# Kernel optimization log

Hardware: AMD Instinct MI355X
Metric: run time of the kernel (lower is better)

The kernel has to match this reference:

```python
import jax, jax.numpy as jnp
import numpy as np

D = 2048        # input_size / model dim
H = 2816        # hidden_size per expert (GLU -> w1 has 2*H rows)
E = 8           # num_experts
M = 4096        # tokens (batch*seq)


def setup_inputs() -> dict:
    key = jax.random.key(0)
    k1, k2, k3, k4, k5 = jax.random.split(key, 5)
    x = jax.random.normal(k1, (M, D), dtype=jnp.float32)
    # ParallelExperts init: uniform(-1/fan_in_dim, 1/fan_in_dim); scale kept simple here
    w1 = jax.random.uniform(k2, (E, 2 * H, D), dtype=jnp.float32, minval=-1.0, maxval=1.0) / (2 * H)
    w2 = jax.random.uniform(k3, (E, D, H), dtype=jnp.float32, minval=-1.0, maxval=1.0) / D
    router_w = jax.random.normal(k4, (E, D), dtype=jnp.float32) * (1.0 / np.sqrt(D))
    bias = jnp.zeros((D,), dtype=jnp.float32)
    return {"x": x, "w1": w1, "w2": w2, "router_w": router_w, "bias": bias, "top_k": 2}


def _moe_forward(x, w1, w2, router_w, bias, top_k):
    # Router: logits -> softmax (fp32) -> top-k -> renormalize (fused_moe semantics)
    logits = x @ router_w.T                                # [M, E]
    probs = jax.nn.softmax(logits.astype(jnp.float32), axis=-1)
    topk_w, topk_ids = jax.lax.top_k(probs, top_k)         # [M, k]
    topk_w = topk_w / jnp.sum(topk_w, axis=-1, keepdims=True)
    # Dense combine weights [M, E]: gate weight if expert selected, else 0
    m = x.shape[0]
    combine = jnp.zeros((m, w1.shape[0]), dtype=x.dtype)
    combine = combine.at[jnp.arange(m)[:, None], topk_ids].add(topk_w.astype(x.dtype))
    # Grouped expert GEMMs, expressed as a loop over the small fixed expert set.
    # Contribution of expert e is masked by combine[:, e] (zero for unrouted tokens).
    y = jnp.zeros_like(x)
    hdim = w2.shape[2]
    for e in range(w1.shape[0]):
        g = x @ w1[e].T                                    # [M, 2H]
        h = jax.nn.silu(g[:, :hdim]) * g[:, hdim:]          # silu_and_mul (GLU)
        y = y + combine[:, e:e + 1] * (h @ w2[e].T)         # [M, D]
    return y + bias


def reference(x, w1, w2, router_w, bias, top_k):
    return _moe_forward(x, w1, w2, router_w, bias, top_k)
```

## Files before the change

kernel.cpp:

```cpp
#include <hip/hip_runtime.h>
#include <hip/hip_bf16.h>
#include <stdint.h>

#define M_TOK 4096
#define DDIM  2048
#define HDIM  2816
#define NEXP  8
#define PMAX  10240
#define MAXTILES 40
#define NB1   22
#define NB2   8
#define NT1   64
#define NT2   88

typedef __attribute__((ext_vector_type(8))) short short8;
typedef __attribute__((ext_vector_type(4))) float f32x4;

#define GLD16(g, l) __builtin_amdgcn_global_load_lds(                              \
    (const __attribute__((address_space(1))) unsigned int*)(g),                    \
    (__attribute__((address_space(3))) unsigned int*)(l), 16, 0, 0)

#define VMCNT(n) asm volatile("s_waitcnt vmcnt(" #n ")" ::: "memory")

__device__ __forceinline__ unsigned short f2bf(float f) {
  unsigned int u = __float_as_uint(f);
  u += 0x7fffu + ((u >> 16) & 1u);
  return (unsigned short)(u >> 16);
}
__device__ __forceinline__ float bf2f(unsigned short u) {
  return __uint_as_float(((unsigned)u) << 16);
}

#define PHASE(TT, VM, STG)                                                       \
  {                                                                              \
    VMCNT(VM);                                                                   \
    __builtin_amdgcn_s_barrier();                                                \
    asm volatile("" ::: "memory");                                               \
    if (STG) {                                                                   \
      int st_ = (TT) + 3;                                                        \
      int t4s_ = st_ & 3;                                                        \
      size_t kb_ = (size_t)st_ * 64;                                             \
      GLD16(aS0 + kb_, ldsp + t4s_ * 16384 + aD0);                               \
      GLD16(aS1 + kb_, ldsp + t4s_ * 16384 + aD1);                               \
      GLD16(bS0 + kb_, ldsp + 65536 + t4s_ * 16384 + aD0);                       \
      GLD16(bS1 + kb_, ldsp + 65536 + t4s_ * 16384 + aD1);                       \
    }                                                                            \
    {                                                                            \
      int t4_ = (TT) & 3;                                                        \
      const char* ab_ = ldsp + t4_ * 16384;                                      \
      const char* bb_ = ldsp + 65536 + t4_ * 16384;                              \
      short8 av_[8], bv_[4];                                                     \
      _Pragma("unroll") for (int mi = 0; mi < 8; ++mi)                           \
        av_[mi] = *(const short8*)(ab_ + aoff[mi]);                              \
      _Pragma("unroll") for (int ni = 0; ni < 4; ++ni)                           \
        bv_[ni] = *(const short8*)(bb_ + boff[ni]);                              \
      __builtin_amdgcn_s_setprio(1);                                             \
      _Pragma("unroll") for (int mi = 0; mi < 8; ++mi)                           \
        _Pragma("unroll") for (int ni = 0; ni < 4; ++ni)                         \
          acc[mi][ni] = __builtin_amdgcn_mfma_f32_16x16x32_bf16(av_[mi], bv_[ni], acc[mi][ni], 0, 0, 0); \
      __builtin_amdgcn_s_setprio(0);                                             \
    }                                                                            \
  }

__global__ void cvt_bf16_k(const float4* __restrict__ in, ushort4* __restrict__ out, int n4) {
  int stride = gridDim.x * blockDim.x;
  for (int i = blockIdx.x * blockDim.x + threadIdx.x; i < n4; i += stride) {
    float4 v = in[i];
    ushort4 o;
    o.x = f2bf(v.x); o.y = f2bf(v.y); o.z = f2bf(v.z); o.w = f2bf(v.w);
    out[i] = o;
  }
}

__global__ void init_k(int* __restrict__ tok, int* __restrict__ counts, int* __restrict__ cursors) {
  int i = blockIdx.x * blockDim.x + threadIdx.x;
  if (i < PMAX) tok[i] = -1;
  if (i < NEXP) { counts[i] = 0; cursors[i] = 0; }
}

__global__ __launch_bounds__(256) void router_k(const float* __restrict__ x,
                                                const float* __restrict__ rw,
                                                float* __restrict__ wgt,
                                                int* __restrict__ eid,
                                                int* __restrict__ counts) {
  int lane = threadIdx.x & 63;
  int wv = threadIdx.x >> 6;
  int t = blockIdx.x * 4 + wv;
  const float* xr = x + (size_t)t * DDIM;
  float acc[NEXP];
#pragma unroll
  for (int e = 0; e < NEXP; ++e) acc[e] = 0.f;
  for (int j = 0; j < DDIM / 64; ++j) {
    float xv = xr[lane + j * 64];
#pragma unroll
    for (int e = 0; e < NEXP; ++e) acc[e] += xv * rw[e * DDIM + lane + j * 64];
  }
#pragma unroll
  for (int e = 0; e < NEXP; ++e) {
#pragma unroll
    for (int s = 32; s > 0; s >>= 1) acc[e] += __shfl_xor(acc[e], s, 64);
  }
  if (lane == 0) {
    float mx = acc[0];
#pragma unroll
    for (int e = 1; e < NEXP; ++e) mx = fmaxf(mx, acc[e]);
    float p[NEXP];
#pragma unroll
    for (int e = 0; e < NEXP; ++e) p[e] = expf(acc[e] - mx);
    int e0 = 0; float p0 = p[0];
#pragma unroll
    for (int e = 1; e < NEXP; ++e) if (p[e] > p0) { p0 = p[e]; e0 = e; }
    int e1 = -1; float p1 = -1.f;
#pragma unroll
    for (int e = 0; e < NEXP; ++e) if (e != e0 && p[e] > p1) { p1 = p[e]; e1 = e; }
    float s = p0 + p1;
    wgt[2 * t] = p0 / s; wgt[2 * t + 1] = p1 / s;
    eid[2 * t] = e0;     eid[2 * t + 1] = e1;
    atomicAdd(&counts[e0], 1);
    atomicAdd(&counts[e1], 1);
  }
}

__global__ void offsets_k(const int* __restrict__ counts, int* __restrict__ offs,
                          int* __restrict__ tile2exp, int* __restrict__ tilerow,
                          int* __restrict__ ntiles) {
  if (threadIdx.x == 0 && blockIdx.x == 0) {
    int o = 0, nt = 0;
    for (int e = 0; e < NEXP; ++e) {
      offs[e] = o;
      int c = counts[e];
      int pt = (c + 255) >> 8;
      for (int i = 0; i < pt; ++i) { tile2exp[nt] = e; tilerow[nt] = o + i * 256; ++nt; }
      o += pt << 8;
    }
    offs[NEXP] = o;
    ntiles[0] = nt;
  }
}

__global__ void scatter_k(const int* __restrict__ eid, const int* __restrict__ offs,
                          int* __restrict__ cursors, int* __restrict__ tok,
                          int* __restrict__ slot) {
  int t = blockIdx.x * blockDim.x + threadIdx.x;
  if (t >= M_TOK) return;
#pragma unroll
  for (int k = 0; k < 2; ++k) {
    int e = eid[2 * t + k];
    int p = offs[e] + atomicAdd(&cursors[e], 1);
    tok[p] = t;
    slot[2 * t + k] = p;
  }
}

__global__ __launch_bounds__(512, 2) void gemm1_k(const unsigned short* __restrict__ xb,
                                                  const unsigned short* __restrict__ w1b,
                                                  const int* __restrict__ tok,
                                                  const int* __restrict__ tile2exp,
                                                  const int* __restrict__ tilerow,
                                                  const int* __restrict__ ntiles,
                                                  unsigned short* __restrict__ h) {
  __shared__ char ldsp[131072];
  int mt = blockIdx.x;
  if (mt >= ntiles[0]) return;
  int e = tile2exp[mt], r0 = tilerow[mt];
  int n0 = blockIdx.y * 128;
  int tid = threadIdx.x, lane = tid & 63;
  int wv = tid >> 6, wm = wv >> 2, wn = wv & 3;
  int l15 = lane & 15, g = lane >> 4;

  int row0 = tid >> 2, g0 = (tid & 3) ^ ((row0 >> 1) & 3);
  int s1i = 512 + tid;
  int row1 = s1i >> 2, g1 = (s1i & 3) ^ ((row1 >> 1) & 3);
  int t0 = tok[r0 + row0]; if (t0 < 0) t0 = 0;
  int t1 = tok[r0 + row1]; if (t1 < 0) t1 = 0;
  const char* aS0 = (const char*)xb + (size_t)t0 * (DDIM * 2) + g0 * 16;
  const char* aS1 = (const char*)xb + (size_t)t1 * (DDIM * 2) + g1 * 16;
  size_t w1r0 = (size_t)e * (2 * HDIM) +
                (row0 < 128 ? (size_t)(n0 + row0) : (size_t)(HDIM + n0 + row0 - 128));
  size_t w1r1 = (size_t)e * (2 * HDIM) +
                (row1 < 128 ? (size_t)(n0 + row1) : (size_t)(HDIM + n0 + row1 - 128));
  const char* bS0 = (const char*)w1b + w1r0 * (DDIM * 2) + g0 * 16;
  const char* bS1 = (const char*)w1b + w1r1 * (DDIM * 2) + g1 * 16;
  int aD0 = tid * 16, aD1 = 8192 + tid * 16;

  int aoff[8], boff[4];
#pragma unroll
  for (int mi = 0; mi < 8; ++mi) {
    int r = wm * 128 + mi * 16 + l15;
    aoff[mi] = r * 64 + ((g ^ ((r >> 1) & 3)) * 16);
  }
#pragma unroll
  for (int ni = 0; ni < 4; ++ni) {
    int r = wn * 64 + ni * 16 + l15;
    boff[ni] = r * 64 + ((g ^ ((r >> 1) & 3)) * 16);
  }

  f32x4 acc[8][4];
#pragma unroll
  for (int mi = 0; mi < 8; ++mi)
#pragma unroll
    for (int ni = 0; ni < 4; ++ni) acc[mi][ni] = (f32x4)(0.f);

#pragma unroll
  for (int t = 0; t < 3; ++t) {
    GLD16(aS0 + (size_t)t * 64, ldsp + t * 16384 + aD0);
    GLD16(aS1 + (size_t)t * 64, ldsp + t * 16384 + aD1);
    GLD16(bS0 + (size_t)t * 64, ldsp + 65536 + t * 16384 + aD0);
    GLD16(bS1 + (size_t)t * 64, ldsp + 65536 + t * 16384 + aD1);
  }

  int T = 0;
  for (; T + 3 < NT1; ++T) PHASE(T, 8, 1);
  PHASE(T, 8, 0); ++T;
  PHASE(T, 4, 0); ++T;
  PHASE(T, 0, 0);

  __syncthreads();
  float* xch = (float*)ldsp;
  int rbase = (lane >> 4) * 4;
  if (wn >= 2) {
    int uc0 = (wn - 2) * 64;
#pragma unroll
    for (int mi = 0; mi < 8; ++mi)
#pragma unroll
      for (int ni = 0; ni < 4; ++ni)
#pragma unroll
        for (int j = 0; j < 4; ++j) {
          int r = wm * 128 + mi * 16 + rbase + j;
          int c = uc0 + ni * 16 + l15;
          xch[r * 128 + c] = acc[mi][ni][j];
        }
  }
  __syncthreads();
  if (wn < 2) {
#pragma unroll
    for (int mi = 0; mi < 8; ++mi)
#pragma unroll
      for (int ni = 0; ni < 4; ++ni)
#pragma unroll
        for (int j = 0; j < 4; ++j) {
          int r = wm * 128 + mi * 16 + rbase + j;
          int c = wn * 64 + ni * 16 + l15;
          float gg = acc[mi][ni][j];
          float u = xch[r * 128 + c];
          float sv = gg / (1.f + expf(-gg));
          h[(size_t)(r0 + r) * HDIM + n0 + c] = f2bf(sv * u);
        }
  }
}

__global__ __launch_bounds__(512, 2) void gemm2_k(const unsigned short* __restrict__ h,
                                                  const unsigned short* __restrict__ w2b,
                                                  const int* __restrict__ tile2exp,
                                                  const int* __restrict__ tilerow,
                                                  const int* __restrict__ ntiles,
                                                  unsigned short* __restrict__ yp) {
  __shared__ char ldsp[131072];
  int mt = blockIdx.x;
  if (mt >= ntiles[0]) return;
  int e = tile2exp[mt], r0 = tilerow[mt];
  int n0 = blockIdx.y * 256;
  int tid = threadIdx.x, lane = tid & 63;
  int wv = tid >> 6, wm = wv >> 2, wn = wv & 3;
  int l15 = lane & 15, g = lane >> 4;

  int row0 = tid >> 2, g0 = (tid & 3) ^ ((row0 >> 1) & 3);
  int s1i = 512 + tid;
  int row1 = s1i >> 2, g1 = (s1i & 3) ^ ((row1 >> 1) & 3);
  const char* aS0 = (const char*)h + (size_t)(r0 + row0) * (HDIM * 2) + g0 * 16;
  const char* aS1 = (const char*)h + (size_t)(r0 + row1) * (HDIM * 2) + g1 * 16;
  const char* bS0 = (const char*)w2b + ((size_t)e * DDIM + n0 + row0) * (HDIM * 2) + g0 * 16;
  const char* bS1 = (const char*)w2b + ((size_t)e * DDIM + n0 + row1) * (HDIM * 2) + g1 * 16;
  int aD0 = tid * 16, aD1 = 8192 + tid * 16;

  int aoff[8], boff[4];
#pragma unroll
  for (int mi = 0; mi < 8; ++mi) {
    int r = wm * 128 + mi * 16 + l15;
    aoff[mi] = r * 64 + ((g ^ ((r >> 1) & 3)) * 16);
  }
#pragma unroll
  for (int ni = 0; ni < 4; ++ni) {
    int r = wn * 64 + ni * 16 + l15;
    boff[ni] = r * 64 + ((g ^ ((r >> 1) & 3)) * 16);
  }

  f32x4 acc[8][4];
#pragma unroll
  for (int mi = 0; mi < 8; ++mi)
#pragma unroll
    for (int ni = 0; ni < 4; ++ni) acc[mi][ni] = (f32x4)(0.f);

#pragma unroll
  for (int t = 0; t < 3; ++t) {
    GLD16(aS0 + (size_t)t * 64, ldsp + t * 16384 + aD0);
    GLD16(aS1 + (size_t)t * 64, ldsp + t * 16384 + aD1);
    GLD16(bS0 + (size_t)t * 64, ldsp + 65536 + t * 16384 + aD0);
    GLD16(bS1 + (size_t)t * 64, ldsp + 65536 + t * 16384 + aD1);
  }

  int T = 0;
  for (; T + 3 < NT2; ++T) PHASE(T, 8, 1);
  PHASE(T, 8, 0); ++T;
  PHASE(T, 4, 0); ++T;
  PHASE(T, 0, 0);

  int rbase = (lane >> 4) * 4;
#pragma unroll
  for (int mi = 0; mi < 8; ++mi)
#pragma unroll
    for (int ni = 0; ni < 4; ++ni)
#pragma unroll
      for (int j = 0; j < 4; ++j) {
        int r = r0 + wm * 128 + mi * 16 + rbase + j;
        int c = n0 + wn * 64 + ni * 16 + l15;
        yp[(size_t)r * DDIM + c] = f2bf(acc[mi][ni][j]);
      }
}

__global__ void combine_k(const unsigned short* __restrict__ yp, const float* __restrict__ wgt,
                          const int* __restrict__ slot, const float* __restrict__ bias,
                          float* __restrict__ out) {
  int idx = blockIdx.x * blockDim.x + threadIdx.x;
  int t = idx >> 8, q = (idx & 255) * 8;
  float w0 = wgt[2 * t], w1 = wgt[2 * t + 1];
  int s0 = slot[2 * t], s1 = slot[2 * t + 1];
  short8 a8 = *(const short8*)(yp + (size_t)s0 * DDIM + q);
  short8 b8 = *(const short8*)(yp + (size_t)s1 * DDIM + q);
  float* op = out + (size_t)t * DDIM + q;
#pragma unroll
  for (int k = 0; k < 8; ++k) {
    float av = bf2f((unsigned short)a8[k]);
    float bv = bf2f((unsigned short)b8[k]);
    op[k] = w0 * av + w1 * bv + bias[q + k];
  }
}

extern "C" void kernel_launch(void* const* d_in, const int* in_sizes, int n_in,
                              void* d_out, int out_size, void* d_ws, size_t ws_size,
                              hipStream_t stream) {
  const float* x    = (const float*)d_in[0];
  const float* w1   = (const float*)d_in[1];
  const float* w2   = (const float*)d_in[2];
  const float* rw   = (const float*)d_in[3];
  const float* bias = (const float*)d_in[4];
  float* out = (float*)d_out;

  char* ws = (char*)d_ws;
  size_t off = 0;
  auto alloc = [&](size_t bytes) -> void* {
    void* p = ws + off;
    off = (off + bytes + 255) & ~(size_t)255;
    return p;
  };
  unsigned short* w1b = (unsigned short*)alloc((size_t)NEXP * 2 * HDIM * DDIM * 2);
  unsigned short* w2b = (unsigned short*)alloc((size_t)NEXP * DDIM * HDIM * 2);
  unsigned short* xb  = (unsigned short*)alloc((size_t)M_TOK * DDIM * 2);
  unsigned short* h   = (unsigned short*)alloc((size_t)PMAX * HDIM * 2);
  unsigned short* yp  = (unsigned short*)alloc((size_t)PMAX * DDIM * 2);
  float* wgt          = (float*)alloc((size_t)M_TOK * 2 * 4);
  int* eid            = (int*)alloc((size_t)M_TOK * 2 * 4);
  int* slot           = (int*)alloc((size_t)M_TOK * 2 * 4);
  int* tok            = (int*)alloc((size_t)PMAX * 4);
  int* counts         = (int*)alloc(64 * 4);
  int* cursors        = (int*)alloc(64 * 4);
  int* offs           = (int*)alloc(64 * 4);
  int* ntiles         = (int*)alloc(64 * 4);
  int* tile2exp       = (int*)alloc(128 * 4);
  int* tilerow        = (int*)alloc(128 * 4);

  hipLaunchKernelGGL(init_k, dim3((PMAX + 255) / 256), dim3(256), 0, stream, tok, counts, cursors);
  hipLaunchKernelGGL(cvt_bf16_k, dim3(2048), dim3(256), 0, stream,
                     (const float4*)w1, (ushort4*)w1b, (int)((size_t)NEXP * 2 * HDIM * DDIM / 4));
  hipLaunchKernelGGL(cvt_bf16_k, dim3(2048), dim3(256), 0, stream,
                     (const float4*)w2, (ushort4*)w2b, (int)((size_t)NEXP * DDIM * HDIM / 4));
  hipLaunchKernelGGL(cvt_bf16_k, dim3(2048), dim3(256), 0, stream,
                     (const float4*)x, (ushort4*)xb, (int)((size_t)M_TOK * DDIM / 4));
  hipLaunchKernelGGL(router_k, dim3(M_TOK / 4), dim3(256), 0, stream, x, rw, wgt, eid, counts);
  hipLaunchKernelGGL(offsets_k, dim3(1), dim3(64), 0, stream, counts, offs, tile2exp, tilerow, ntiles);
  hipLaunchKernelGGL(scatter_k, dim3((M_TOK + 255) / 256), dim3(256), 0, stream, eid, offs, cursors, tok, slot);
  hipLaunchKernelGGL(gemm1_k, dim3(MAXTILES, NB1), dim3(512), 0, stream, xb, w1b, tok, tile2exp, tilerow, ntiles, h);
  hipLaunchKernelGGL(gemm2_k, dim3(MAXTILES, NB2), dim3(512), 0, stream, h, w2b, tile2exp, tilerow, ntiles, yp);
  hipLaunchKernelGGL(combine_k, dim3(M_TOK * (DDIM / 8) / 256), dim3(256), 0, stream, yp, wgt, slot, bias, out);
}
```

Baseline: 763.5 us.

## Fuse x conversion into router, overlap w2 conversion with gemm1, retile gemm2

The router kernel now writes the bf16 copy of x itself, which removes a separate conversion pass over x. The fp32-to-bf16 conversion of w2 moves into extra blocks of the gemm1 grid so it runs alongside the first GEMM. Both GEMMs get register double-buffered LDS reads under a sched_barrier, and occupancy drops to one block per CU. gemm2 uses 128-row tiles, giving twice as many tiles and less LDS per block. The gemm1 epilogue exchange buffer gets an XOR swizzle to reduce bank conflicts. The risks are that the conversion blocks compete with GEMM blocks for CUs and that the lower occupancy cannot hide latency as well.

Result: no change. 752.0 us (-1.5%).

```diff
diff --git a/kernel.cpp b/kernel.cpp
--- a/kernel.cpp
+++ b/kernel.cpp
@@ -8,7 +8,9 @@
 #define NEXP  8
 #define PMAX  10240
 #define MAXTILES 40
+#define CVW   8
 #define NB1   22
+#define MAXT2 80
 #define NB2   8
 #define NT1   64
 #define NT2   88
@@ -30,37 +32,6 @@
 __device__ __forceinline__ float bf2f(unsigned short u) {
   return __uint_as_float(((unsigned)u) << 16);
 }
-
-#define PHASE(TT, VM, STG)                                                       \
-  {                                                                              \
-    VMCNT(VM);                                                                   \
-    __builtin_amdgcn_s_barrier();                                                \
-    asm volatile("" ::: "memory");                                               \
-    if (STG) {                                                                   \
-      int st_ = (TT) + 3;                                                        \
-      int t4s_ = st_ & 3;                                                        \
-      size_t kb_ = (size_t)st_ * 64;                                             \
-      GLD16(aS0 + kb_, ldsp + t4s_ * 16384 + aD0);                               \
-      GLD16(aS1 + kb_, ldsp + t4s_ * 16384 + aD1);                               \
-      GLD16(bS0 + kb_, ldsp + 65536 + t4s_ * 16384 + aD0);                       \
-      GLD16(bS1 + kb_, ldsp + 65536 + t4s_ * 16384 + aD1);                       \
-    }                                                                            \
-    {                                                                            \
-      int t4_ = (TT) & 3;                                                        \
-      const char* ab_ = ldsp + t4_ * 16384;                                      \
-      const char* bb_ = ldsp + 65536 + t4_ * 16384;                              \
-      short8 av_[8], bv_[4];                                                     \
-      _Pragma("unroll") for (int mi = 0; mi < 8; ++mi)                           \
-        av_[mi] = *(const short8*)(ab_ + aoff[mi]);                              \
-      _Pragma("unroll") for (int ni = 0; ni < 4; ++ni)                           \
-        bv_[ni] = *(const short8*)(bb_ + boff[ni]);                              \
-      __builtin_amdgcn_s_setprio(1);                                             \
-      _Pragma("unroll") for (int mi = 0; mi < 8; ++mi)                           \
-        _Pragma("unroll") for (int ni = 0; ni < 4; ++ni)                         \
-          acc[mi][ni] = __builtin_amdgcn_mfma_f32_16x16x32_bf16(av_[mi], bv_[ni], acc[mi][ni], 0, 0, 0); \
-      __builtin_amdgcn_s_setprio(0);                                             \
-    }                                                                            \
-  }
 
 __global__ void cvt_bf16_k(const float4* __restrict__ in, ushort4* __restrict__ out, int n4) {
   int stride = gridDim.x * blockDim.x;
@@ -78,22 +49,30 @@
   if (i < NEXP) { counts[i] = 0; cursors[i] = 0; }
 }
 
-__global__ __launch_bounds__(256) void router_k(const float* __restrict__ x,
-                                                const float* __restrict__ rw,
+__global__ __launch_bounds__(256) void router_k(const float4* __restrict__ x4,
+                                                const float4* __restrict__ rw4,
+                                                ushort4* __restrict__ xb4,
                                                 float* __restrict__ wgt,
                                                 int* __restrict__ eid,
                                                 int* __restrict__ counts) {
   int lane = threadIdx.x & 63;
   int wv = threadIdx.x >> 6;
   int t = blockIdx.x * 4 + wv;
-  const float* xr = x + (size_t)t * DDIM;
+  int base = t * (DDIM / 4);
   float acc[NEXP];
 #pragma unroll
   for (int e = 0; e < NEXP; ++e) acc[e] = 0.f;
-  for (int j = 0; j < DDIM / 64; ++j) {
-    float xv = xr[lane + j * 64];
-#pragma unroll
-    for (int e = 0; e < NEXP; ++e) acc[e] += xv * rw[e * DDIM + lane + j * 64];
+#pragma unroll
+  for (int j = 0; j < DDIM / 4 / 64; ++j) {
+    float4 v = x4[base + j * 64 + lane];
+    ushort4 o;
+    o.x = f2bf(v.x); o.y = f2bf(v.y); o.z = f2bf(v.z); o.w = f2bf(v.w);
+    xb4[base + j * 64 + lane] = o;
+#pragma unroll
+    for (int e = 0; e < NEXP; ++e) {
+      float4 w = rw4[e * (DDIM / 4) + j * 64 + lane];
+      acc[e] += v.x * w.x + v.y * w.y + v.z * w.z + v.w * w.w;
+    }
   }
 #pragma unroll
   for (int e = 0; e < NEXP; ++e) {
@@ -123,18 +102,25 @@
 
 __global__ void offsets_k(const int* __restrict__ counts, int* __restrict__ offs,
                           int* __restrict__ tile2exp, int* __restrict__ tilerow,
-                          int* __restrict__ ntiles) {
+                          int* __restrict__ ntiles,
+                          int* __restrict__ tile2exp2, int* __restrict__ tilerow2,
+                          int* __restrict__ ntiles2) {
   if (threadIdx.x == 0 && blockIdx.x == 0) {
-    int o = 0, nt = 0;
+    int o = 0, nt = 0, nt2 = 0;
     for (int e = 0; e < NEXP; ++e) {
       offs[e] = o;
       int c = counts[e];
       int pt = (c + 255) >> 8;
-      for (int i = 0; i < pt; ++i) { tile2exp[nt] = e; tilerow[nt] = o + i * 256; ++nt; }
+      for (int i = 0; i < pt; ++i) {
+        tile2exp[nt] = e; tilerow[nt] = o + i * 256; ++nt;
+        tile2exp2[nt2] = e; tilerow2[nt2] = o + i * 256; ++nt2;
+        tile2exp2[nt2] = e; tilerow2[nt2] = o + i * 256 + 128; ++nt2;
+      }
       o += pt << 8;
     }
     offs[NEXP] = o;
     ntiles[0] = nt;
+    ntiles2[0] = nt2;
   }
 }
 
@@ -152,15 +138,62 @@
   }
 }
 
-__global__ __launch_bounds__(512, 2) void gemm1_k(const unsigned short* __restrict__ xb,
+#define STAGE1(TT)                                                               \
+  { size_t kb_ = (size_t)(TT) * 64;                                              \
+    char* d_ = ldsp + ((TT) & 3) * 16384;                                        \
+    GLD16(aS0 + kb_, d_ + aD0);                                                  \
+    GLD16(aS1 + kb_, d_ + aD1);                                                  \
+    GLD16(bS0 + kb_, d_ + 65536 + aD0);                                          \
+    GLD16(bS1 + kb_, d_ + 65536 + aD1); }
+
+#define DSRD1(TT, AV, BV)                                                        \
+  { const char* ab_ = ldsp + ((TT) & 3) * 16384;                                 \
+    const char* bb_ = ab_ + 65536;                                               \
+    _Pragma("unroll") for (int mi = 0; mi < 8; ++mi)                             \
+      AV[mi] = *(const short8*)(ab_ + aoff[mi]);                                 \
+    _Pragma("unroll") for (int ni = 0; ni < 4; ++ni)                             \
+      BV[ni] = *(const short8*)(bb_ + boff[ni]); }
+
+#define MMA1(AV, BV)                                                             \
+  { __builtin_amdgcn_s_setprio(1);                                               \
+    _Pragma("unroll") for (int mi = 0; mi < 8; ++mi)                             \
+      _Pragma("unroll") for (int ni = 0; ni < 4; ++ni)                           \
+        acc[mi][ni] = __builtin_amdgcn_mfma_f32_16x16x32_bf16(AV[mi], BV[ni], acc[mi][ni], 0, 0, 0); \
+    __builtin_amdgcn_s_setprio(0); }
+
+#define BODY1(TT, VMN, STG, AVC, BVC, AVN, BVN, RD)                              \
+  { VMCNT(VMN);                                                                  \
+    __builtin_amdgcn_s_barrier();                                                \
+    asm volatile("" ::: "memory");                                               \
+    if (STG) STAGE1((TT) + 3);                                                   \
+    if (RD) DSRD1((TT) + 1, AVN, BVN);                                           \
+    __builtin_amdgcn_sched_barrier(0);                                           \
+    MMA1(AVC, BVC); }
+
+__global__ __launch_bounds__(512, 1) void gemm1_k(const unsigned short* __restrict__ xb,
                                                   const unsigned short* __restrict__ w1b,
                                                   const int* __restrict__ tok,
                                                   const int* __restrict__ tile2exp,
                                                   const int* __restrict__ tilerow,
                                                   const int* __restrict__ ntiles,
-                                                  unsigned short* __restrict__ h) {
+                                                  unsigned short* __restrict__ h,
+                                                  const float4* __restrict__ w2src,
+                                                  ushort4* __restrict__ w2b4) {
   __shared__ char ldsp[131072];
-  int mt = blockIdx.x;
+  int bx = blockIdx.x;
+  if (bx >= MAXTILES) {
+    int id = (bx - MAXTILES) * NB1 + blockIdx.y;
+    const int n4 = NEXP * DDIM * HDIM / 4;
+    const int stride = CVW * NB1 * 512;
+    for (int i = id * 512 + threadIdx.x; i < n4; i += stride) {
+      float4 v = w2src[i];
+      ushort4 o;
+      o.x = f2bf(v.x); o.y = f2bf(v.y); o.z = f2bf(v.z); o.w = f2bf(v.w);
+      w2b4[i] = o;
+    }
+    return;
+  }
+  int mt = bx;
   if (mt >= ntiles[0]) return;
   int e = tile2exp[mt], r0 = tilerow[mt];
   int n0 = blockIdx.y * 128;
@@ -201,19 +234,24 @@
 #pragma unroll
     for (int ni = 0; ni < 4; ++ni) acc[mi][ni] = (f32x4)(0.f);
 
-#pragma unroll
-  for (int t = 0; t < 3; ++t) {
-    GLD16(aS0 + (size_t)t * 64, ldsp + t * 16384 + aD0);
-    GLD16(aS1 + (size_t)t * 64, ldsp + t * 16384 + aD1);
-    GLD16(bS0 + (size_t)t * 64, ldsp + 65536 + t * 16384 + aD0);
-    GLD16(bS1 + (size_t)t * 64, ldsp + 65536 + t * 16384 + aD1);
-  }
-
-  int T = 0;
-  for (; T + 3 < NT1; ++T) PHASE(T, 8, 1);
-  PHASE(T, 8, 0); ++T;
-  PHASE(T, 4, 0); ++T;
-  PHASE(T, 0, 0);
+  short8 avA[8], bvA[4], avB[8], bvB[4];
+
+  STAGE1(0); STAGE1(1); STAGE1(2);
+  VMCNT(8);
+  __builtin_amdgcn_s_barrier();
+  asm volatile("" ::: "memory");
+  DSRD1(0, avA, bvA);
+
+  for (int T = 0; T < NT1 - 4; T += 4) {
+    BODY1(T + 0, 4, 1, avA, bvA, avB, bvB, 1);
+    BODY1(T + 1, 4, 1, avB, bvB, avA, bvA, 1);
+    BODY1(T + 2, 4, 1, avA, bvA, avB, bvB, 1);
+    BODY1(T + 3, 4, 1, avB, bvB, avA, bvA, 1);
+  }
+  BODY1(NT1 - 4, 4, 1, avA, bvA, avB, bvB, 1);
+  BODY1(NT1 - 3, 4, 0, avB, bvB, avA, bvA, 1);
+  BODY1(NT1 - 2, 0, 0, avA, bvA, avB, bvB, 1);
+  BODY1(NT1 - 1, 0, 0, avB, bvB, avA, bvA, 0);
 
   __syncthreads();
   float* xch = (float*)ldsp;
@@ -228,7 +266,8 @@
         for (int j = 0; j < 4; ++j) {
           int r = wm * 128 + mi * 16 + rbase + j;
           int c = uc0 + ni * 16 + l15;
-          xch[r * 128 + c] = acc[mi][ni][j];
+          int cs = c ^ ((r & 3) << 2) ^ ((r & 1) << 4);
+          xch[r * 128 + cs] = acc[mi][ni][j];
         }
   }
   __syncthreads();
@@ -241,42 +280,73 @@
         for (int j = 0; j < 4; ++j) {
           int r = wm * 128 + mi * 16 + rbase + j;
           int c = wn * 64 + ni * 16 + l15;
+          int cs = c ^ ((r & 3) << 2) ^ ((r & 1) << 4);
           float gg = acc[mi][ni][j];
-          float u = xch[r * 128 + c];
+          float u = xch[r * 128 + cs];
           float sv = gg / (1.f + expf(-gg));
           h[(size_t)(r0 + r) * HDIM + n0 + c] = f2bf(sv * u);
         }
   }
 }
 
-__global__ __launch_bounds__(512, 2) void gemm2_k(const unsigned short* __restrict__ h,
+#define STAGE2(TT)                                                               \
+  { size_t kb_ = (size_t)(TT) * 64;                                              \
+    GLD16(aS0 + kb_, ldsp + ((TT) & 3) * 8192 + aD0);                            \
+    GLD16(bS0 + kb_, ldsp + 32768 + ((TT) & 3) * 16384 + bD0);                   \
+    GLD16(bS1 + kb_, ldsp + 32768 + ((TT) & 3) * 16384 + bD1); }
+
+#define DSRD2(TT, AV, BV)                                                        \
+  { const char* ab_ = ldsp + ((TT) & 3) * 8192;                                  \
+    const char* bb_ = ldsp + 32768 + ((TT) & 3) * 16384;                         \
+    _Pragma("unroll") for (int mi = 0; mi < 4; ++mi)                             \
+      AV[mi] = *(const short8*)(ab_ + aoff[mi]);                                 \
+    _Pragma("unroll") for (int ni = 0; ni < 4; ++ni)                             \
+      BV[ni] = *(const short8*)(bb_ + boff[ni]); }
+
+#define MMA2(AV, BV)                                                             \
+  { __builtin_amdgcn_s_setprio(1);                                               \
+    _Pragma("unroll") for (int mi = 0; mi < 4; ++mi)                             \
+      _Pragma("unroll") for (int ni = 0; ni < 4; ++ni)                           \
+        acc[mi][ni] = __builtin_amdgcn_mfma_f32_16x16x32_bf16(AV[mi], BV[ni], acc[mi][ni], 0, 0, 0); \
+    __builtin_amdgcn_s_setprio(0); }
+
+#define BODY2(TT, VMN, STG, AVC, BVC, AVN, BVN, RD)                              \
+  { VMCNT(VMN);                                                                  \
+    __builtin_amdgcn_s_barrier();                                                \
+    asm volatile("" ::: "memory");                                               \
+    if (STG) STAGE2((TT) + 3);                                                   \
+    if (RD) DSRD2((TT) + 1, AVN, BVN);                                           \
+    __builtin_amdgcn_sched_barrier(0);                                           \
+    MMA2(AVC, BVC); }
+
+__global__ __launch_bounds__(512, 1) void gemm2_k(const unsigned short* __restrict__ h,
                                                   const unsigned short* __restrict__ w2b,
-                                                  const int* __restrict__ tile2exp,
-                                                  const int* __restrict__ tilerow,
-                                                  const int* __restrict__ ntiles,
+                                                  const int* __restrict__ tile2exp2,
+                                                  const int* __restrict__ tilerow2,
+                                                  const int* __restrict__ ntiles2,
                                                   unsigned short* __restrict__ yp) {
-  __shared__ char ldsp[131072];
+  __shared__ char ldsp[98304];
   int mt = blockIdx.x;
-  if (mt >= ntiles[0]) return;
-  int e = tile2exp[mt], r0 = tilerow[mt];
+  if (mt >= ntiles2[0]) return;
+  int e = tile2exp2[mt], r0 = tilerow2[mt];
   int n0 = blockIdx.y * 256;
   int tid = threadIdx.x, lane = tid & 63;
   int wv = tid >> 6, wm = wv >> 2, wn = wv & 3;
   int l15 = lane & 15, g = lane >> 4;
 
-  int row0 = tid >> 2, g0 = (tid & 3) ^ ((row0 >> 1) & 3);
+  int rowa = tid >> 2, ga = (tid & 3) ^ ((rowa >> 1) & 3);
+  int rb0 = tid >> 2, gb0 = (tid & 3) ^ ((rb0 >> 1) & 3);
   int s1i = 512 + tid;
-  int row1 = s1i >> 2, g1 = (s1i & 3) ^ ((row1 >> 1) & 3);
-  const char* aS0 = (const char*)h + (size_t)(r0 + row0) * (HDIM * 2) + g0 * 16;
-  const char* aS1 = (const char*)h + (size_t)(r0 + row1) * (HDIM * 2) + g1 * 16;
-  const char* bS0 = (const char*)w2b + ((size_t)e * DDIM + n0 + row0) * (HDIM * 2) + g0 * 16;
-  const char* bS1 = (const char*)w2b + ((size_t)e * DDIM + n0 + row1) * (HDIM * 2) + g1 * 16;
-  int aD0 = tid * 16, aD1 = 8192 + tid * 16;
-
-  int aoff[8], boff[4];
-#pragma unroll
-  for (int mi = 0; mi < 8; ++mi) {
-    int r = wm * 128 + mi * 16 + l15;
+  int rb1 = s1i >> 2, gb1 = (s1i & 3) ^ ((rb1 >> 1) & 3);
+  const char* aS0 = (const char*)h + (size_t)(r0 + rowa) * (HDIM * 2) + ga * 16;
+  const char* bS0 = (const char*)w2b + ((size_t)e * DDIM + n0 + rb0) * (HDIM * 2) + gb0 * 16;
+  const char* bS1 = (const char*)w2b + ((size_t)e * DDIM + n0 + rb1) * (HDIM * 2) + gb1 * 16;
+  int aD0 = tid * 16, bD0 = tid * 16, bD1 = 8192 + tid * 16;
+
+  int aoff[4], boff[4];
+#pragma unroll
+  for (int mi = 0; mi < 4; ++mi) {
+    int r = wm * 64 + mi * 16 + l15;
     aoff[mi] = r * 64 + ((g ^ ((r >> 1) & 3)) * 16);
   }
 #pragma unroll
@@ -285,34 +355,39 @@
     boff[ni] = r * 64 + ((g ^ ((r >> 1) & 3)) * 16);
   }
 
-  f32x4 acc[8][4];
-#pragma unroll
-  for (int mi = 0; mi < 8; ++mi)
+  f32x4 acc[4][4];
+#pragma unroll
+  for (int mi = 0; mi < 4; ++mi)
 #pragma unroll
     for (int ni = 0; ni < 4; ++ni) acc[mi][ni] = (f32x4)(0.f);
 
-#pragma unroll
-  for (int t = 0; t < 3; ++t) {
-    GLD16(aS0 + (size_t)t * 64, ldsp + t * 16384 + aD0);
-    GLD16(aS1 + (size_t)t * 64, ldsp + t * 16384 + aD1);
-    GLD16(bS0 + (size_t)t * 64, ldsp + 65536 + t * 16384 + aD0);
-    GLD16(bS1 + (size_t)t * 64, ldsp + 65536 + t * 16384 + aD1);
-  }
-
-  int T = 0;
-  for (; T + 3 < NT2; ++T) PHASE(T, 8, 1);
-  PHASE(T, 8, 0); ++T;
-  PHASE(T, 4, 0); ++T;
-  PHASE(T, 0, 0);
+  short8 avA[4], bvA[4], avB[4], bvB[4];
+
+  STAGE2(0); STAGE2(1); STAGE2(2);
+  VMCNT(6);
+  __builtin_amdgcn_s_barrier();
+  asm volatile("" ::: "memory");
+  DSRD2(0, avA, bvA);
+
+  for (int T = 0; T < NT2 - 4; T += 4) {
+    BODY2(T + 0, 3, 1, avA, bvA, avB, bvB, 1);
+    BODY2(T + 1, 3, 1, avB, bvB, avA, bvA, 1);
+    BODY2(T + 2, 3, 1, avA, bvA, avB, bvB, 1);
+    BODY2(T + 3, 3, 1, avB, bvB, avA, bvA, 1);
+  }
+  BODY2(NT2 - 4, 3, 1, avA, bvA, avB, bvB, 1);
+  BODY2(NT2 - 3, 3, 0, avB, bvB, avA, bvA, 1);
+  BODY2(NT2 - 2, 0, 0, avA, bvA, avB, bvB, 1);
+  BODY2(NT2 - 1, 0, 0, avB, bvB, avA, bvA, 0);
 
   int rbase = (lane >> 4) * 4;
 #pragma unroll
-  for (int mi = 0; mi < 8; ++mi)
+  for (int mi = 0; mi < 4; ++mi)
 #pragma unroll
     for (int ni = 0; ni < 4; ++ni)
 #pragma unroll
       for (int j = 0; j < 4; ++j) {
-        int r = r0 + wm * 128 + mi * 16 + rbase + j;
+        int r = r0 + wm * 64 + mi * 16 + rbase + j;
         int c = n0 + wn * 64 + ni * 16 + l15;
         yp[(size_t)r * DDIM + c] = f2bf(acc[mi][ni][j]);
       }
@@ -366,20 +441,23 @@
   int* cursors        = (int*)alloc(64 * 4);
   int* offs           = (int*)alloc(64 * 4);
   int* ntiles         = (int*)alloc(64 * 4);
+  int* ntiles2        = (int*)alloc(64 * 4);
   int* tile2exp       = (int*)alloc(128 * 4);
   int* tilerow        = (int*)alloc(128 * 4);
+  int* tile2exp2      = (int*)alloc(128 * 4);
+  int* tilerow2       = (int*)alloc(128 * 4);
 
   hipLaunchKernelGGL(init_k, dim3((PMAX + 255) / 256), dim3(256), 0, stream, tok, counts, cursors);
   hipLaunchKernelGGL(cvt_bf16_k, dim3(2048), dim3(256), 0, stream,
                      (const float4*)w1, (ushort4*)w1b, (int)((size_t)NEXP * 2 * HDIM * DDIM / 4));
-  hipLaunchKernelGGL(cvt_bf16_k, dim3(2048), dim3(256), 0, stream,
-                     (const float4*)w2, (ushort4*)w2b, (int)((size_t)NEXP * DDIM * HDIM / 4));
-  hipLaunchKernelGGL(cvt_bf16_k, dim3(2048), dim3(256), 0, stream,
-                     (const float4*)x, (ushort4*)xb, (int)((size_t)M_TOK * DDIM / 4));
-  hipLaunchKernelGGL(router_k, dim3(M_TOK / 4), dim3(256), 0, stream, x, rw, wgt, eid, counts);
-  hipLaunchKernelGGL(offsets_k, dim3(1), dim3(64), 0, stream, counts, offs, tile2exp, tilerow, ntiles);
+  hipLaunchKernelGGL(router_k, dim3(M_TOK / 4), dim3(256), 0, stream,
+                     (const float4*)x, (const float4*)rw, (ushort4*)xb, wgt, eid, counts);
+  hipLaunchKernelGGL(offsets_k, dim3(1), dim3(64), 0, stream, counts, offs,
+                     tile2exp, tilerow, ntiles, tile2exp2, tilerow2, ntiles2);
   hipLaunchKernelGGL(scatter_k, dim3((M_TOK + 255) / 256), dim3(256), 0, stream, eid, offs, cursors, tok, slot);
-  hipLaunchKernelGGL(gemm1_k, dim3(MAXTILES, NB1), dim3(512), 0, stream, xb, w1b, tok, tile2exp, tilerow, ntiles, h);
-  hipLaunchKernelGGL(gemm2_k, dim3(MAXTILES, NB2), dim3(512), 0, stream, h, w2b, tile2exp, tilerow, ntiles, yp);
+  hipLaunchKernelGGL(gemm1_k, dim3(MAXTILES + CVW, NB1), dim3(512), 0, stream,
+                     xb, w1b, tok, tile2exp, tilerow, ntiles, h, (const float4*)w2, (ushort4*)w2b);
+  hipLaunchKernelGGL(gemm2_k, dim3(MAXT2, NB2), dim3(512), 0, stream,
+                     h, w2b, tile2exp2, tilerow2, ntiles2, yp);
   hipLaunchKernelGGL(combine_k, dim3(M_TOK * (DDIM / 8) / 256), dim3(256), 0, stream, yp, wgt, slot, bias, out);
 }
```

## Split GEMM k-steps into two half-phases, fuse x cast into router, swizzle exchange

Applied to the files above, without the earlier changes.

Each GEMM k-step is split into two barrier-separated half-phases. The first loads half the A fragments and all B fragments and issues the A prefetch. The second loads the other A half and issues the B prefetch. This interleaves global-to-LDS traffic with MFMA work and cuts live fragment registers, while launch bounds drop to one block per SM. The separate x-to-bf16 conversion kernel is folded into the router kernel, which now reads float4, saving a full pass over x. The GLU exchange buffer in LDS gets an XOR column swizzle to reduce bank conflicts, at the cost of twice as many barriers per k-step.

Result: no change. 757.2 us (-0.8%).

```diff
diff --git a/kernel.cpp b/kernel.cpp
--- a/kernel.cpp
+++ b/kernel.cpp
@@ -31,36 +31,45 @@
   return __uint_as_float(((unsigned)u) << 16);
 }
 
-#define PHASE(TT, VM, STG)                                                       \
-  {                                                                              \
-    VMCNT(VM);                                                                   \
+#define GP0(KT, VM, STG)                                                         \
+  { VMCNT(VM);                                                                   \
     __builtin_amdgcn_s_barrier();                                                \
     asm volatile("" ::: "memory");                                               \
-    if (STG) {                                                                   \
-      int st_ = (TT) + 3;                                                        \
-      int t4s_ = st_ & 3;                                                        \
-      size_t kb_ = (size_t)st_ * 64;                                             \
-      GLD16(aS0 + kb_, ldsp + t4s_ * 16384 + aD0);                               \
-      GLD16(aS1 + kb_, ldsp + t4s_ * 16384 + aD1);                               \
-      GLD16(bS0 + kb_, ldsp + 65536 + t4s_ * 16384 + aD0);                       \
-      GLD16(bS1 + kb_, ldsp + 65536 + t4s_ * 16384 + aD1);                       \
+    { const char* ab_ = ldsp + ((KT) & 3) * 16384;                               \
+      const char* bb_ = ldsp + 65536 + ((KT) & 3) * 16384;                       \
+      _Pragma("unroll") for (int mi = 0; mi < 4; ++mi)                           \
+        av[mi] = *(const short8*)(ab_ + aoff[mi]);                               \
+      _Pragma("unroll") for (int ni = 0; ni < 4; ++ni)                           \
+        bv[ni] = *(const short8*)(bb_ + boff[ni]);                               \
+      if (STG) { size_t kb_ = (size_t)((KT) + 3) * 64;                           \
+        char* d_ = ldsp + (((KT) + 3) & 3) * 16384;                              \
+        GLD16(aS0 + kb_, d_ + aD0); GLD16(aS1 + kb_, d_ + aD1); }                \
     }                                                                            \
-    {                                                                            \
-      int t4_ = (TT) & 3;                                                        \
-      const char* ab_ = ldsp + t4_ * 16384;                                      \
-      const char* bb_ = ldsp + 65536 + t4_ * 16384;                              \
-      short8 av_[8], bv_[4];                                                     \
-      _Pragma("unroll") for (int mi = 0; mi < 8; ++mi)                           \
-        av_[mi] = *(const short8*)(ab_ + aoff[mi]);                              \
+    asm volatile("" ::: "memory");                                               \
+    __builtin_amdgcn_s_barrier();                                                \
+    __builtin_amdgcn_s_setprio(1);                                               \
+    _Pragma("unroll") for (int mi = 0; mi < 4; ++mi)                             \
       _Pragma("unroll") for (int ni = 0; ni < 4; ++ni)                           \
-        bv_[ni] = *(const short8*)(bb_ + boff[ni]);                              \
-      __builtin_amdgcn_s_setprio(1);                                             \
-      _Pragma("unroll") for (int mi = 0; mi < 8; ++mi)                           \
-        _Pragma("unroll") for (int ni = 0; ni < 4; ++ni)                         \
-          acc[mi][ni] = __builtin_amdgcn_mfma_f32_16x16x32_bf16(av_[mi], bv_[ni], acc[mi][ni], 0, 0, 0); \
-      __builtin_amdgcn_s_setprio(0);                                             \
+        acc[mi][ni] = __builtin_amdgcn_mfma_f32_16x16x32_bf16(av[mi], bv[ni], acc[mi][ni], 0, 0, 0); \
+    __builtin_amdgcn_s_setprio(0); }
+
+#define GP1(KT, STG)                                                             \
+  { __builtin_amdgcn_s_barrier();                                                \
+    asm volatile("" ::: "memory");                                               \
+    { const char* ab_ = ldsp + ((KT) & 3) * 16384;                               \
+      _Pragma("unroll") for (int mi = 0; mi < 4; ++mi)                           \
+        av[mi] = *(const short8*)(ab_ + aoff[4 + mi]);                           \
+      if (STG) { size_t kb_ = (size_t)((KT) + 3) * 64;                           \
+        char* d_ = ldsp + 65536 + (((KT) + 3) & 3) * 16384;                      \
+        GLD16(bS0 + kb_, d_ + aD0); GLD16(bS1 + kb_, d_ + aD1); }                \
     }                                                                            \
-  }
+    asm volatile("" ::: "memory");                                               \
+    __builtin_amdgcn_s_barrier();                                                \
+    __builtin_amdgcn_s_setprio(1);                                               \
+    _Pragma("unroll") for (int mi = 0; mi < 4; ++mi)                             \
+      _Pragma("unroll") for (int ni = 0; ni < 4; ++ni)                           \
+        acc[4 + mi][ni] = __builtin_amdgcn_mfma_f32_16x16x32_bf16(av[mi], bv[ni], acc[4 + mi][ni], 0, 0, 0); \
+    __builtin_amdgcn_s_setprio(0); }
 
 __global__ void cvt_bf16_k(const float4* __restrict__ in, ushort4* __restrict__ out, int n4) {
   int stride = gridDim.x * blockDim.x;
@@ -78,22 +87,30 @@
   if (i < NEXP) { counts[i] = 0; cursors[i] = 0; }
 }
 
-__global__ __launch_bounds__(256) void router_k(const float* __restrict__ x,
-                                                const float* __restrict__ rw,
+__global__ __launch_bounds__(256) void router_k(const float4* __restrict__ x4,
+                                                const float4* __restrict__ rw4,
+                                                ushort4* __restrict__ xb4,
                                                 float* __restrict__ wgt,
                                                 int* __restrict__ eid,
                                                 int* __restrict__ counts) {
   int lane = threadIdx.x & 63;
   int wv = threadIdx.x >> 6;
   int t = blockIdx.x * 4 + wv;
-  const float* xr = x + (size_t)t * DDIM;
+  int base = t * (DDIM / 4);
   float acc[NEXP];
 #pragma unroll
   for (int e = 0; e < NEXP; ++e) acc[e] = 0.f;
-  for (int j = 0; j < DDIM / 64; ++j) {
-    float xv = xr[lane + j * 64];
-#pragma unroll
-    for (int e = 0; e < NEXP; ++e) acc[e] += xv * rw[e * DDIM + lane + j * 64];
+#pragma unroll
+  for (int j = 0; j < DDIM / 4 / 64; ++j) {
+    float4 v = x4[base + j * 64 + lane];
+    ushort4 o;
+    o.x = f2bf(v.x); o.y = f2bf(v.y); o.z = f2bf(v.z); o.w = f2bf(v.w);
+    xb4[base + j * 64 + lane] = o;
+#pragma unroll
+    for (int e = 0; e < NEXP; ++e) {
+      float4 w = rw4[e * (DDIM / 4) + j * 64 + lane];
+      acc[e] += v.x * w.x + v.y * w.y + v.z * w.z + v.w * w.w;
+    }
   }
 #pragma unroll
   for (int e = 0; e < NEXP; ++e) {
@@ -152,7 +169,7 @@
   }
 }
 
-__global__ __launch_bounds__(512, 2) void gemm1_k(const unsigned short* __restrict__ xb,
+__global__ __launch_bounds__(512, 1) void gemm1_k(const unsigned short* __restrict__ xb,
                                                   const unsigned short* __restrict__ w1b,
                                                   const int* __restrict__ tok,
                                                   const int* __restrict__ tile2exp,
@@ -169,18 +186,16 @@
   int l15 = lane & 15, g = lane >> 4;
 
   int row0 = tid >> 2, g0 = (tid & 3) ^ ((row0 >> 1) & 3);
-  int s1i = 512 + tid;
-  int row1 = s1i >> 2, g1 = (s1i & 3) ^ ((row1 >> 1) & 3);
+  int row1 = row0 + 128;
   int t0 = tok[r0 + row0]; if (t0 < 0) t0 = 0;
   int t1 = tok[r0 + row1]; if (t1 < 0) t1 = 0;
   const char* aS0 = (const char*)xb + (size_t)t0 * (DDIM * 2) + g0 * 16;
-  const char* aS1 = (const char*)xb + (size_t)t1 * (DDIM * 2) + g1 * 16;
+  const char* aS1 = (const char*)xb + (size_t)t1 * (DDIM * 2) + g0 * 16;
   size_t w1r0 = (size_t)e * (2 * HDIM) +
                 (row0 < 128 ? (size_t)(n0 + row0) : (size_t)(HDIM + n0 + row0 - 128));
-  size_t w1r1 = (size_t)e * (2 * HDIM) +
-                (row1 < 128 ? (size_t)(n0 + row1) : (size_t)(HDIM + n0 + row1 - 128));
+  size_t w1r1 = (size_t)e * (2 * HDIM) + (size_t)(HDIM + n0 + row1 - 128);
   const char* bS0 = (const char*)w1b + w1r0 * (DDIM * 2) + g0 * 16;
-  const char* bS1 = (const char*)w1b + w1r1 * (DDIM * 2) + g1 * 16;
+  const char* bS1 = (const char*)w1b + w1r1 * (DDIM * 2) + g0 * 16;
   int aD0 = tid * 16, aD1 = 8192 + tid * 16;
 
   int aoff[8], boff[4];
@@ -200,6 +215,8 @@
   for (int mi = 0; mi < 8; ++mi)
 #pragma unroll
     for (int ni = 0; ni < 4; ++ni) acc[mi][ni] = (f32x4)(0.f);
+
+  short8 av[4], bv[4];
 
 #pragma unroll
   for (int t = 0; t < 3; ++t) {
@@ -209,11 +226,10 @@
     GLD16(bS1 + (size_t)t * 64, ldsp + 65536 + t * 16384 + aD1);
   }
 
-  int T = 0;
-  for (; T + 3 < NT1; ++T) PHASE(T, 8, 1);
-  PHASE(T, 8, 0); ++T;
-  PHASE(T, 4, 0); ++T;
-  PHASE(T, 0, 0);
+  for (int kt = 0; kt < NT1 - 3; ++kt) { GP0(kt, 8, 1); GP1(kt, 1); }
+  GP0(NT1 - 3, 8, 0); GP1(NT1 - 3, 0);
+  GP0(NT1 - 2, 4, 0); GP1(NT1 - 2, 0);
+  GP0(NT1 - 1, 0, 0); GP1(NT1 - 1, 0);
 
   __syncthreads();
   float* xch = (float*)ldsp;
@@ -228,7 +244,8 @@
         for (int j = 0; j < 4; ++j) {
           int r = wm * 128 + mi * 16 + rbase + j;
           int c = uc0 + ni * 16 + l15;
-          xch[r * 128 + c] = acc[mi][ni][j];
+          int cs = c ^ ((r & 3) << 2) ^ ((r & 1) << 4);
+          xch[r * 128 + cs] = acc[mi][ni][j];
         }
   }
   __syncthreads();
@@ -241,15 +258,16 @@
         for (int j = 0; j < 4; ++j) {
           int r = wm * 128 + mi * 16 + rbase + j;
           int c = wn * 64 + ni * 16 + l15;
+          int cs = c ^ ((r & 3) << 2) ^ ((r & 1) << 4);
           float gg = acc[mi][ni][j];
-          float u = xch[r * 128 + c];
+          float u = xch[r * 128 + cs];
           float sv = gg / (1.f + expf(-gg));
           h[(size_t)(r0 + r) * HDIM + n0 + c] = f2bf(sv * u);
         }
   }
 }
 
-__global__ __launch_bounds__(512, 2) void gemm2_k(const unsigned short* __restrict__ h,
+__global__ __launch_bounds__(512, 1) void gemm2_k(const unsigned short* __restrict__ h,
                                                   const unsigned short* __restrict__ w2b,
                                                   const int* __restrict__ tile2exp,
                                                   const int* __restrict__ tilerow,
@@ -265,12 +283,11 @@
   int l15 = lane & 15, g = lane >> 4;
 
   int row0 = tid >> 2, g0 = (tid & 3) ^ ((row0 >> 1) & 3);
-  int s1i = 512 + tid;
-  int row1 = s1i >> 2, g1 = (s1i & 3) ^ ((row1 >> 1) & 3);
+  int row1 = row0 + 128;
   const char* aS0 = (const char*)h + (size_t)(r0 + row0) * (HDIM * 2) + g0 * 16;
-  const char* aS1 = (const char*)h + (size_t)(r0 + row1) * (HDIM * 2) + g1 * 16;
+  const char* aS1 = (const char*)h + (size_t)(r0 + row1) * (HDIM * 2) + g0 * 16;
   const char* bS0 = (const char*)w2b + ((size_t)e * DDIM + n0 + row0) * (HDIM * 2) + g0 * 16;
-  const char* bS1 = (const char*)w2b + ((size_t)e * DDIM + n0 + row1) * (HDIM * 2) + g1 * 16;
+  const char* bS1 = (const char*)w2b + ((size_t)e * DDIM + n0 + row1) * (HDIM * 2) + g0 * 16;
   int aD0 = tid * 16, aD1 = 8192 + tid * 16;
 
   int aoff[8], boff[4];
@@ -290,6 +307,8 @@
   for (int mi = 0; mi < 8; ++mi)
 #pragma unroll
     for (int ni = 0; ni < 4; ++ni) acc[mi][ni] = (f32x4)(0.f);
+
+  short8 av[4], bv[4];
 
 #pragma unroll
   for (int t = 0; t < 3; ++t) {
@@ -299,11 +318,10 @@
     GLD16(bS1 + (size_t)t * 64, ldsp + 65536 + t * 16384 + aD1);
   }
 
-  int T = 0;
-  for (; T + 3 < NT2; ++T) PHASE(T, 8, 1);
-  PHASE(T, 8, 0); ++T;
-  PHASE(T, 4, 0); ++T;
-  PHASE(T, 0, 0);
+  for (int kt = 0; kt < NT2 - 3; ++kt) { GP0(kt, 8, 1); GP1(kt, 1); }
+  GP0(NT2 - 3, 8, 0); GP1(NT2 - 3, 0);
+  GP0(NT2 - 2, 4, 0); GP1(NT2 - 2, 0);
+  GP0(NT2 - 1, 0, 0); GP1(NT2 - 1, 0);
 
   int rbase = (lane >> 4) * 4;
 #pragma unroll
@@ -374,12 +392,14 @@
                      (const float4*)w1, (ushort4*)w1b, (int)((size_t)NEXP * 2 * HDIM * DDIM / 4));
   hipLaunchKernelGGL(cvt_bf16_k, dim3(2048), dim3(256), 0, stream,
                      (const float4*)w2, (ushort4*)w2b, (int)((size_t)NEXP * DDIM * HDIM / 4));
-  hipLaunchKernelGGL(cvt_bf16_k, dim3(2048), dim3(256), 0, stream,
-                     (const float4*)x, (ushort4*)xb, (int)((size_t)M_TOK * DDIM / 4));
-  hipLaunchKernelGGL(router_k, dim3(M_TOK / 4), dim3(256), 0, stream, x, rw, wgt, eid, counts);
-  hipLaunchKernelGGL(offsets_k, dim3(1), dim3(64), 0, stream, counts, offs, tile2exp, tilerow, ntiles);
+  hipLaunchKernelGGL(router_k, dim3(M_TOK / 4), dim3(256), 0, stream,
+                     (const float4*)x, (const float4*)rw, (ushort4*)xb, wgt, eid, counts);
+  hipLaunchKernelGGL(offsets_k, dim3(1), dim3(64), 0, stream, counts, offs,
+                     tile2exp, tilerow, ntiles);
   hipLaunchKernelGGL(scatter_k, dim3((M_TOK + 255) / 256), dim3(256), 0, stream, eid, offs, cursors, tok, slot);
-  hipLaunchKernelGGL(gemm1_k, dim3(MAXTILES, NB1), dim3(512), 0, stream, xb, w1b, tok, tile2exp, tilerow, ntiles, h);
-  hipLaunchKernelGGL(gemm2_k, dim3(MAXTILES, NB2), dim3(512), 0, stream, h, w2b, tile2exp, tilerow, ntiles, yp);
+  hipLaunchKernelGGL(gemm1_k, dim3(MAXTILES, NB1), dim3(512), 0, stream,
+                     xb, w1b, tok, tile2exp, tilerow, ntiles, h);
+  hipLaunchKernelGGL(gemm2_k, dim3(MAXTILES, NB2), dim3(512), 0, stream,
+                     h, w2b, tile2exp, tilerow, ntiles, yp);
   hipLaunchKernelGGL(combine_k, dim3(M_TOK * (DDIM / 8) / 256), dim3(256), 0, stream, yp, wgt, slot, bias, out);
 }
```
